# Performance work log

Measured on AMD Instinct MI355X. Metric: run time of the kernel, lower is better.

Reference implementation:

```python
import jax, jax.numpy as jnp
import numpy as np

N_NODES = 50000
N_EDGES = 800000
NODE_DIM = 128
EDGE_DIM = 16
OUT_DIM = 64
HEADS = 4


def setup_inputs() -> dict:
    key = jax.random.key(0)
    ks = jax.random.split(key, 12)
    x = jax.random.normal(ks[0], (N_NODES, NODE_DIM), jnp.float32)
    edge_index = jax.random.randint(ks[1], (2, N_EDGES), 0, N_NODES)
    batch = jnp.zeros((N_NODES,), jnp.int32)
    edge_attr = jax.random.normal(ks[2], (N_EDGES, EDGE_DIM), jnp.float32)
    s = 1.0 / np.sqrt(NODE_DIM)
    W = jax.random.normal(ks[3], (NODE_DIM, HEADS * OUT_DIM), jnp.float32) * s
    att_src = jax.random.normal(ks[4], (HEADS, OUT_DIM), jnp.float32) * 0.1
    att_dst = jax.random.normal(ks[5], (HEADS, OUT_DIM), jnp.float32) * 0.1
    W_e = jax.random.normal(ks[6], (EDGE_DIM, HEADS * OUT_DIM), jnp.float32) * (1.0 / np.sqrt(EDGE_DIM))
    att_edge = jax.random.normal(ks[7], (HEADS, OUT_DIM), jnp.float32) * 0.1
    bias = jnp.zeros((OUT_DIM,), jnp.float32)
    gamma = jnp.ones((OUT_DIM,), jnp.float32)
    beta = jnp.zeros((OUT_DIM,), jnp.float32)
    return {"x": x, "edge_index": edge_index, "batch": batch, "edge_attr": edge_attr,
            "W": W, "att_src": att_src, "att_dst": att_dst, "W_e": W_e,
            "att_edge": att_edge, "bias": bias, "gamma": gamma, "beta": beta}


def reference(x, edge_index, batch, edge_attr, W, att_src, att_dst, W_e, att_edge, bias, gamma, beta):
    N = x.shape[0]
    H, C = att_src.shape
    src, dst = edge_index[0], edge_index[1]
    E = src.shape[0]

    # add self loops; self-loop edge_attr = per-node mean of incoming edge attrs (PyG fill_value='mean')
    cnt = jax.ops.segment_sum(jnp.ones((E, 1), x.dtype), dst, num_segments=N)
    loop_attr = jax.ops.segment_sum(edge_attr, dst, num_segments=N) / jnp.maximum(cnt, 1.0)
    loop_idx = jnp.arange(N, dtype=src.dtype)
    src_f = jnp.concatenate([src, loop_idx])
    dst_f = jnp.concatenate([dst, loop_idx])
    ea = jnp.concatenate([edge_attr, loop_attr], axis=0)

    h = (x @ W).reshape(N, H, C)                       # [N,H,C]
    a_src = jnp.einsum('nhc,hc->nh', h, att_src)       # [N,H]
    a_dst = jnp.einsum('nhc,hc->nh', h, att_dst)
    e_emb = (ea @ W_e).reshape(-1, H, C)               # [E',H,C]
    a_edge = jnp.einsum('ehc,hc->eh', e_emb, att_edge)

    alpha = jax.nn.leaky_relu(a_src[src_f] + a_dst[dst_f] + a_edge, 0.2)  # [E',H]
    amax = jax.ops.segment_max(alpha, dst_f, num_segments=N)
    expa = jnp.exp(alpha - amax[dst_f])
    denom = jax.ops.segment_sum(expa, dst_f, num_segments=N)
    att = expa / (denom[dst_f] + 1e-16)                # segment softmax over dst

    msg = h[src_f] * att[:, :, None]                   # [E',H,C]
    out = jax.ops.segment_sum(msg, dst_f, num_segments=N)  # [N,H,C]
    out = out.mean(axis=1) + bias                      # concat=False -> head mean

    mu = out.mean(-1, keepdims=True)
    var = out.var(-1, keepdims=True)
    out = (out - mu) / jnp.sqrt(var + 1e-5) * gamma + beta
    return jax.nn.elu(out)
```

## Files before the change

### kernel.cpp

```cpp
#include <hip/hip_runtime.h>

typedef unsigned int u32;
typedef unsigned short u16;

static constexpr int NN  = 50000;
static constexpr int EE  = 800000;
static constexpr int CAP = 64;

typedef __attribute__((ext_vector_type(8))) short bf16x8;
typedef __attribute__((ext_vector_type(4))) float f32x4;

__device__ inline float u2f(u32 u){ union{u32 i; float f;} v; v.i=u; return v.f; }
__device__ inline float bf2f(u16 u){ return u2f(((u32)u)<<16); }
__device__ inline u16 f2bf(float f){ union{float f; u32 i;} v; v.f=f; u32 i=v.i;
    return (u16)((i + 0x7fffu + ((i>>16)&1u))>>16); }
__device__ inline float lrelu(float x){ return x > 0.f ? x : 0.2f*x; }

__device__ inline float ld(const void* base, size_t i, int f32m){
    return f32m ? ((const float*)base)[i] : bf2f(((const u16*)base)[i]);
}

__device__ inline float wsum(float v){
    #pragma unroll
    for (int m=1;m<64;m<<=1) v += __shfl_xor(v, m, 64);
    return v;
}
__device__ inline float wmax(float v){
    #pragma unroll
    for (int m=1;m<64;m<<=1) v = fmaxf(v, __shfl_xor(v, m, 64));
    return v;
}

__device__ inline int detect_f32(const u16* xraw){
    int lane = threadIdx.x & 63;
    bool bad = false;
    #pragma unroll
    for (int i = 0; i < 8; ++i){
        float v = bf2f(xraw[2*(lane + i*64)]);
        if (!(fabsf(v) < 1e10f)) bad = true;
    }
    return __any(bad) ? 1 : 0;
}

__global__ __launch_bounds__(256) void k_prep(const u16* __restrict__ xraw,
                                              const void* __restrict__ W,
                                              const void* __restrict__ att_src,
                                              const void* __restrict__ att_dst,
                                              const void* __restrict__ W_e,
                                              const void* __restrict__ att_edge,
                                              int* __restrict__ flag,
                                              u16* __restrict__ Wt,
                                              float* __restrict__ Mv){
    int f32m = detect_f32(xraw);
    int b = blockIdx.x, t = threadIdx.x;
    if (b == 0){
        if (t == 0) *flag = f32m;
        if (t < 64){
            int d = t >> 2, h = t & 3;
            float s = 0.f;
            for (int c = 0; c < 64; ++c)
                s += ld(W_e, d*256 + h*64 + c, f32m) * ld(att_edge, h*64 + c, f32m);
            Mv[t] = s;
        }
    } else if (b <= 128){
        int i = (b-1)*256 + t;
        int k = i >> 8, n = i & 255;
        Wt[n*128 + k] = f2bf(ld(W, (size_t)k*256 + n, f32m));
    } else {
        int i = (b-129)*256 + t;
        int c = i >> 7, k = i & 127;
        float s = 0.f;
        if (c < 8){
            int h = c & 3;
            const void* att = (c < 4) ? att_src : att_dst;
            for (int j = 0; j < 64; ++j)
                s += ld(W, (size_t)k*256 + h*64 + j, f32m) * ld(att, h*64 + j, f32m);
        }
        Wt[(size_t)(256 + c)*128 + k] = f2bf(s);
    }
}

__global__ __launch_bounds__(256) void k_edge(const int* __restrict__ ei,
                                              const void* __restrict__ ea,
                                              const float* __restrict__ Mv,
                                              const int* __restrict__ flag,
                                              int* __restrict__ deg,
                                              int* __restrict__ bsrc,
                                              uint2* __restrict__ bae, int E){
    __shared__ float Ml[64];
    if (threadIdx.x < 64) Ml[threadIdx.x] = Mv[threadIdx.x];
    __syncthreads();
    int e = blockIdx.x*256 + threadIdx.x;
    if (e >= E) return;
    int f32m = *flag;
    float v[16];
    if (f32m){
        const float4* r = ((const float4*)ea) + (size_t)e*4;
        float4 a = r[0], b = r[1], c = r[2], d = r[3];
        v[0]=a.x; v[1]=a.y; v[2]=a.z; v[3]=a.w;
        v[4]=b.x; v[5]=b.y; v[6]=b.z; v[7]=b.w;
        v[8]=c.x; v[9]=c.y; v[10]=c.z; v[11]=c.w;
        v[12]=d.x; v[13]=d.y; v[14]=d.z; v[15]=d.w;
    } else {
        const uint4* r = ((const uint4*)ea) + (size_t)e*2;
        uint4 q0 = r[0], q1 = r[1];
        v[0]=u2f(q0.x<<16); v[1]=u2f(q0.x&0xffff0000u);
        v[2]=u2f(q0.y<<16); v[3]=u2f(q0.y&0xffff0000u);
        v[4]=u2f(q0.z<<16); v[5]=u2f(q0.z&0xffff0000u);
        v[6]=u2f(q0.w<<16); v[7]=u2f(q0.w&0xffff0000u);
        v[8]=u2f(q1.x<<16); v[9]=u2f(q1.x&0xffff0000u);
        v[10]=u2f(q1.y<<16); v[11]=u2f(q1.y&0xffff0000u);
        v[12]=u2f(q1.z<<16); v[13]=u2f(q1.z&0xffff0000u);
        v[14]=u2f(q1.w<<16); v[15]=u2f(q1.w&0xffff0000u);
    }
    float a0=0,a1=0,a2=0,a3=0;
    #pragma unroll
    for (int j = 0; j < 16; ++j){
        a0 = fmaf(v[j], Ml[j*4+0], a0);
        a1 = fmaf(v[j], Ml[j*4+1], a1);
        a2 = fmaf(v[j], Ml[j*4+2], a2);
        a3 = fmaf(v[j], Ml[j*4+3], a3);
    }
    int src = ei[e], dst = ei[E + e];
    int slot = atomicAdd(&deg[dst], 1);
    if (slot < CAP){
        bsrc[dst*CAP + slot] = src;
        u32 lo = (u32)f2bf(a0) | ((u32)f2bf(a1)<<16);
        u32 hi = (u32)f2bf(a2) | ((u32)f2bf(a3)<<16);
        bae[dst*CAP + slot] = make_uint2(lo, hi);
    }
}

static constexpr int LDSROW = 136;
static constexpr int CROW   = 264;

__global__ __launch_bounds__(256) void k_gemm(const void* __restrict__ x,
                                              const u16* __restrict__ Wt,
                                              const int* __restrict__ flag,
                                              u16* __restrict__ hbuf,
                                              float* __restrict__ a_src,
                                              float* __restrict__ a_dst, int N){
    __shared__ u16 sh[64*CROW];
    int f32m = *flag;
    int t = threadIdx.x;
    int row0 = blockIdx.x*64;
    if (f32m){
        const float4* xg = (const float4*)x;
        #pragma unroll
        for (int j=0;j<8;++j){
            int idx = t + j*256;
            int r = idx >> 5, c4 = idx & 31;
            int gr = row0 + r; if (gr >= N) gr = N-1;
            float4 v = xg[(size_t)gr*32 + c4];
            u32 p0 = (u32)f2bf(v.x) | ((u32)f2bf(v.y)<<16);
            u32 p1 = (u32)f2bf(v.z) | ((u32)f2bf(v.w)<<16);
            *(uint2*)&sh[r*LDSROW + c4*4] = make_uint2(p0,p1);
        }
    } else {
        const uint4* xg = (const uint4*)x;
        #pragma unroll
        for (int j=0;j<4;++j){
            int idx = t + j*256;
            int r = idx >> 4, c8 = idx & 15;
            int gr = row0 + r; if (gr >= N) gr = N-1;
            uint4 v = xg[(size_t)gr*16 + c8];
            *(uint4*)&sh[r*LDSROW + c8*8] = v;
        }
    }
    __syncthreads();
    int wave = t >> 6, lane = t & 63;
    int l15 = lane & 15, quad = lane >> 4;
    int mrow = wave*16 + l15;
    bf16x8 afr[4];
    #pragma unroll
    for (int s=0;s<4;++s)
        afr[s] = *(const bf16x8*)&sh[mrow*LDSROW + s*32 + quad*8];
    __syncthreads();
    f32x4 acc[17];
    #pragma unroll
    for (int tl=0;tl<17;++tl){
        f32x4 a = {0.f,0.f,0.f,0.f};
        #pragma unroll
        for (int s=0;s<4;++s){
            bf16x8 bfr = *(const bf16x8*)&Wt[(size_t)(tl*16 + l15)*128 + s*32 + quad*8];
            a = __builtin_amdgcn_mfma_f32_16x16x32_bf16(afr[s], bfr, a, 0, 0, 0);
        }
        acc[tl] = a;
    }
    int rbase = row0 + wave*16 + quad*4;
    #pragma unroll
    for (int r=0;r<4;++r){
        int gr = rbase + r;
        if (gr < N){
            if (l15 < 4)      a_src[gr*4 + l15]     = acc[16][r];
            else if (l15 < 8) a_dst[gr*4 + (l15-4)] = acc[16][r];
        }
    }
    #pragma unroll
    for (int r=0;r<4;++r){
        int row = wave*16 + quad*4 + r;
        #pragma unroll
        for (int tl=0;tl<4;++tl){
            u32 lo = (u32)f2bf(acc[tl  ][r]) | ((u32)f2bf(acc[tl+4 ][r])<<16);
            u32 hi = (u32)f2bf(acc[tl+8][r]) | ((u32)f2bf(acc[tl+12][r])<<16);
            *(uint2*)&sh[row*CROW + (tl*16 + l15)*4] = make_uint2(lo, hi);
        }
    }
    __syncthreads();
    uint4* h4 = (uint4*)hbuf;
    #pragma unroll
    for (int j=0;j<8;++j){
        int idx = t + j*256;
        int row = idx >> 5, c16 = idx & 31;
        if (row0 + row < N){
            uint4 v = *(const uint4*)&sh[row*CROW + c16*8];
            h4[(size_t)(row0 + row)*32 + c16] = v;
        }
    }
}

__device__ inline void accum8(float* acc, float4 w, uint4 v){
    acc[0] = fmaf(w.x, u2f(v.x<<16),         acc[0]);
    acc[1] = fmaf(w.y, u2f(v.x&0xffff0000u), acc[1]);
    acc[2] = fmaf(w.z, u2f(v.y<<16),         acc[2]);
    acc[3] = fmaf(w.w, u2f(v.y&0xffff0000u), acc[3]);
    acc[4] = fmaf(w.x, u2f(v.z<<16),         acc[4]);
    acc[5] = fmaf(w.y, u2f(v.z&0xffff0000u), acc[5]);
    acc[6] = fmaf(w.z, u2f(v.w<<16),         acc[6]);
    acc[7] = fmaf(w.w, u2f(v.w&0xffff0000u), acc[7]);
}

__global__ __launch_bounds__(256) void k_node(const int* __restrict__ deg,
                                              const int* __restrict__ bsrc,
                                              const uint2* __restrict__ bae,
                                              const float* __restrict__ a_src,
                                              const float* __restrict__ a_dst,
                                              const u16* __restrict__ hbuf,
                                              const void* __restrict__ bias,
                                              const void* __restrict__ gamma,
                                              const void* __restrict__ beta,
                                              const int* __restrict__ flag,
                                              void* __restrict__ out, int N){
    __shared__ float4 wls[4][CAP+2];
    __shared__ int    sls[4][CAP+2];
    int f32m = *flag;
    int lane = threadIdx.x & 63;
    int slot = threadIdx.x >> 6;
    int n = blockIdx.x*4 + slot;
    int dg = deg[n];
    int dc = dg < CAP ? dg : CAP;
    const float4* as4 = (const float4*)a_src;
    float4 ad = ((const float4*)a_dst)[n];
    float4 an = as4[n];
    bool v0 = lane < dc;
    int s0 = n;
    float ae[4] = {0.f,0.f,0.f,0.f};
    float al0[4] = {-1e30f,-1e30f,-1e30f,-1e30f};
    if (v0){
        s0 = bsrc[n*CAP + lane];
        uint2 p = bae[n*CAP + lane];
        ae[0] = u2f(p.x<<16); ae[1] = u2f(p.x&0xffff0000u);
        ae[2] = u2f(p.y<<16); ae[3] = u2f(p.y&0xffff0000u);
        float4 as = as4[s0];
        al0[0] = lrelu(as.x + ad.x + ae[0]);
        al0[1] = lrelu(as.y + ad.y + ae[1]);
        al0[2] = lrelu(as.z + ad.z + ae[2]);
        al0[3] = lrelu(as.w + ad.w + ae[3]);
    }
    float invd = 1.f / (float)(dg > 1 ? dg : 1);
    float aS[4];
    #pragma unroll
    for (int h=0;h<4;++h) aS[h] = wsum(ae[h]) * invd;
    float alS[4];
    alS[0] = lrelu(an.x + ad.x + aS[0]);
    alS[1] = lrelu(an.y + ad.y + aS[1]);
    alS[2] = lrelu(an.z + ad.z + aS[2]);
    alS[3] = lrelu(an.w + ad.w + aS[3]);
    float ex0[4], exS[4], inv[4];
    #pragma unroll
    for (int h = 0; h < 4; ++h){
        float mx = fmaxf(wmax(al0[h]), alS[h]);
        ex0[h] = v0 ? expf(al0[h] - mx) : 0.f;
        exS[h] = expf(alS[h] - mx);
        float s = wsum(ex0[h]) + exS[h];
        inv[h] = 1.f / (s + 1e-16f);
    }
    if (v0){
        wls[slot][lane] = make_float4(ex0[0]*inv[0], ex0[1]*inv[1], ex0[2]*inv[2], ex0[3]*inv[3]);
        sls[slot][lane] = s0;
    }
    if (lane == 0){
        wls[slot][dc]   = make_float4(exS[0]*inv[0], exS[1]*inv[1], exS[2]*inv[2], exS[3]*inv[3]);
        sls[slot][dc]   = n;
        wls[slot][dc+1] = make_float4(0.f,0.f,0.f,0.f);
        sls[slot][dc+1] = n;
    }
    __syncthreads();
    int T = dc + 1;
    int pairs = (T + 1) >> 1;
    int half = lane >> 5, l5 = lane & 31;
    const uint4* hb4 = (const uint4*)hbuf;
    float acc[8] = {0,0,0,0,0,0,0,0};
    int t = 0;
    for (; t + 2 <= pairs; t += 2){
        int ja = 2*t + half, jb = 2*t + 2 + half;
        int sa = sls[slot][ja], sb = sls[slot][jb];
        float4 wa = wls[slot][ja], wb = wls[slot][jb];
        uint4 va = hb4[(size_t)sa*32 + l5];
        uint4 vb = hb4[(size_t)sb*32 + l5];
        accum8(acc, wa, va);
        accum8(acc, wb, vb);
    }
    for (; t < pairs; ++t){
        int j = 2*t + half;
        int s = sls[slot][j];
        float4 w = wls[slot][j];
        uint4 v = hb4[(size_t)s*32 + l5];
        accum8(acc, w, v);
    }
    float oc0 = 0.25f*(acc[0]+acc[1]+acc[2]+acc[3]);
    float oc1 = 0.25f*(acc[4]+acc[5]+acc[6]+acc[7]);
    oc0 += __shfl_xor(oc0, 32, 64);
    oc1 += __shfl_xor(oc1, 32, 64);
    float va = __shfl(oc0, lane>>1, 64);
    float vb = __shfl(oc1, lane>>1, 64);
    float o = ((lane & 1) ? vb : va) + ld(bias, lane, f32m);
    float mu = wsum(o) * (1.f/64.f);
    float d = o - mu;
    float var = wsum(d*d) * (1.f/64.f);
    float y = d * rsqrtf(var + 1e-5f) * ld(gamma, lane, f32m) + ld(beta, lane, f32m);
    y = y > 0.f ? y : expf(y) - 1.f;
    if (f32m) ((float*)out)[(size_t)n*64 + lane] = y;
    else      ((u16*)out)[(size_t)n*64 + lane] = f2bf(y);
}

extern "C" void kernel_launch(void* const* d_in, const int* in_sizes, int n_in,
                              void* d_out, int out_size, void* d_ws, size_t ws_size,
                              hipStream_t stream){
    const void* x        = d_in[0];
    const int*  ei       = (const int*)d_in[1];
    const void* ea       = d_in[3];
    const void* W        = d_in[4];
    const void* att_src  = d_in[5];
    const void* att_dst  = d_in[6];
    const void* W_e      = d_in[7];
    const void* att_edge = d_in[8];
    const void* bias     = d_in[9];
    const void* gamma    = d_in[10];
    const void* beta     = d_in[11];
    const int N = NN, E = EE;

    char* p = (char*)d_ws;
    auto alloc = [&](size_t bytes){ void* r = (void*)p; p += (bytes + 255) & ~(size_t)255; return r; };
    int*   deg   = (int*)  alloc((size_t)N*4);
    int*   bsrc  = (int*)  alloc((size_t)N*CAP*4);
    uint2* bae   = (uint2*)alloc((size_t)N*CAP*8);
    float* Mv    = (float*)alloc(64*4);
    float* a_src = (float*)alloc((size_t)N*16);
    float* a_dst = (float*)alloc((size_t)N*16);
    u16*   hbuf  = (u16*)  alloc((size_t)N*256*2);
    u16*   Wt    = (u16*)  alloc((size_t)272*128*2);
    int*   flag  = (int*)  alloc(256);

    hipMemsetAsync(deg, 0, (size_t)N*4, stream);
    k_prep<<<137, 256, 0, stream>>>((const u16*)x, W, att_src, att_dst, W_e, att_edge,
                                    flag, Wt, Mv);
    k_edge<<<(E+255)/256, 256, 0, stream>>>(ei, ea, Mv, flag, deg, bsrc, bae, E);
    k_gemm<<<(N+63)/64, 256, 0, stream>>>(x, Wt, flag, hbuf, a_src, a_dst, N);
    k_node<<<N/4, 256, 0, stream>>>(deg, bsrc, bae, a_src, a_dst, hbuf,
                                    bias, gamma, beta, flag, d_out, N);
}
```

Measured before the change: 305.6 us.

## Compute unnormalized softmax weights per edge with atomic denominators, simplify node aggregation

Reorders the kernels so the node GEMM runs before the edge pass. The edge kernel then computes exp(leaky_relu) attention weights directly, without subtracting a max. It accumulates per-destination denominators and edge-attribute sums with float atomics and stores packed src and bf16 weight records. The node kernel drops its wave-wide max and sum reductions, rescales the stored weights, and aggregates with bf16 dot2 instructions. The trade is removing the segment-max stabilization and reduction work at the cost of eight scattered float atomics per edge, plus possible overflow for large logits.

```diff
diff --git a/kernel.cpp b/kernel.cpp
--- a/kernel.cpp
+++ b/kernel.cpp
@@ -14,6 +14,7 @@
 __device__ inline float bf2f(u16 u){ return u2f(((u32)u)<<16); }
 __device__ inline u16 f2bf(float f){ union{float f; u32 i;} v; v.f=f; u32 i=v.i;
     return (u16)((i + 0x7fffu + ((i>>16)&1u))>>16); }
+__device__ inline u32 pk2(float a, float b){ return (u32)f2bf(a) | ((u32)f2bf(b)<<16); }
 __device__ inline float lrelu(float x){ return x > 0.f ? x : 0.2f*x; }
 
 __device__ inline float ld(const void* base, size_t i, int f32m){
@@ -25,10 +26,26 @@
     for (int m=1;m<64;m<<=1) v += __shfl_xor(v, m, 64);
     return v;
 }
-__device__ inline float wmax(float v){
-    #pragma unroll
-    for (int m=1;m<64;m<<=1) v = fmaxf(v, __shfl_xor(v, m, 64));
-    return v;
+
+#if defined(__has_builtin)
+#if __has_builtin(__builtin_amdgcn_fdot2_f32_bf16)
+#define HAS_DOT2 1
+#endif
+#endif
+
+#ifdef HAS_DOT2
+typedef __attribute__((ext_vector_type(2))) __bf16 bf16x2;
+#endif
+
+__device__ inline float dot2acc(u32 hv, u32 wv, float acc){
+#ifdef HAS_DOT2
+    union { u32 u; bf16x2 v; } a, b; a.u = hv; b.u = wv;
+    return __builtin_amdgcn_fdot2_f32_bf16(a.v, b.v, acc, false);
+#else
+    acc = fmaf(u2f(hv<<16),         u2f(wv<<16),         acc);
+    acc = fmaf(u2f(hv&0xffff0000u), u2f(wv&0xffff0000u), acc);
+    return acc;
+#endif
 }
 
 __device__ inline int detect_f32(const u16* xraw){
@@ -80,13 +97,102 @@
     }
 }
 
+static constexpr int LDSROW = 136;
+static constexpr int CROW   = 264;
+
+__global__ __launch_bounds__(256) void k_gemm(const void* __restrict__ x,
+                                              const u16* __restrict__ Wt,
+                                              const int* __restrict__ flag,
+                                              u16* __restrict__ hbuf,
+                                              float* __restrict__ a_src,
+                                              float* __restrict__ a_dst, int N){
+    __shared__ u16 sh[64*CROW];
+    int f32m = *flag;
+    int t = threadIdx.x;
+    int row0 = blockIdx.x*64;
+    if (f32m){
+        const float4* xg = (const float4*)x;
+        #pragma unroll
+        for (int j=0;j<8;++j){
+            int idx = t + j*256;
+            int r = idx >> 5, c4 = idx & 31;
+            int gr = row0 + r; if (gr >= N) gr = N-1;
+            float4 v = xg[(size_t)gr*32 + c4];
+            *(uint2*)&sh[r*LDSROW + c4*4] = make_uint2(pk2(v.x,v.y), pk2(v.z,v.w));
+        }
+    } else {
+        const uint4* xg = (const uint4*)x;
+        #pragma unroll
+        for (int j=0;j<4;++j){
+            int idx = t + j*256;
+            int r = idx >> 4, c8 = idx & 15;
+            int gr = row0 + r; if (gr >= N) gr = N-1;
+            uint4 v = xg[(size_t)gr*16 + c8];
+            *(uint4*)&sh[r*LDSROW + c8*8] = v;
+        }
+    }
+    __syncthreads();
+    int wave = t >> 6, lane = t & 63;
+    int l15 = lane & 15, quad = lane >> 4;
+    int mrow = wave*16 + l15;
+    bf16x8 afr[4];
+    #pragma unroll
+    for (int s=0;s<4;++s)
+        afr[s] = *(const bf16x8*)&sh[mrow*LDSROW + s*32 + quad*8];
+    __syncthreads();
+    f32x4 acc[17];
+    #pragma unroll
+    for (int tl=0;tl<17;++tl){
+        f32x4 a = {0.f,0.f,0.f,0.f};
+        #pragma unroll
+        for (int s=0;s<4;++s){
+            bf16x8 bfr = *(const bf16x8*)&Wt[(size_t)(tl*16 + l15)*128 + s*32 + quad*8];
+            a = __builtin_amdgcn_mfma_f32_16x16x32_bf16(afr[s], bfr, a, 0, 0, 0);
+        }
+        acc[tl] = a;
+    }
+    int rbase = row0 + wave*16 + quad*4;
+    #pragma unroll
+    for (int r=0;r<4;++r){
+        int gr = rbase + r;
+        if (gr < N){
+            if (l15 < 4)      a_src[gr*4 + l15]     = acc[16][r];
+            else if (l15 < 8) a_dst[gr*4 + (l15-4)] = acc[16][r];
+        }
+    }
+    #pragma unroll
+    for (int r=0;r<4;++r){
+        int row = wave*16 + quad*4 + r;
+        #pragma unroll
+        for (int tl=0;tl<4;++tl){
+            u32 lo = pk2(acc[tl  ][r], acc[tl+4 ][r]);
+            u32 hi = pk2(acc[tl+8][r], acc[tl+12][r]);
+            *(uint2*)&sh[row*CROW + (tl*16 + l15)*4] = make_uint2(lo, hi);
+        }
+    }
+    __syncthreads();
+    uint4* h4 = (uint4*)hbuf;
+    #pragma unroll
+    for (int j=0;j<8;++j){
+        int idx = t + j*256;
+        int row = idx >> 5, c16 = idx & 31;
+        if (row0 + row < N){
+            uint4 v = *(const uint4*)&sh[row*CROW + c16*8];
+            h4[(size_t)(row0 + row)*32 + c16] = v;
+        }
+    }
+}
+
 __global__ __launch_bounds__(256) void k_edge(const int* __restrict__ ei,
                                               const void* __restrict__ ea,
                                               const float* __restrict__ Mv,
                                               const int* __restrict__ flag,
+                                              const float* __restrict__ a_src,
+                                              const float* __restrict__ a_dst,
                                               int* __restrict__ deg,
-                                              int* __restrict__ bsrc,
-                                              uint2* __restrict__ bae, int E){
+                                              float* __restrict__ denom,
+                                              float* __restrict__ aesum,
+                                              uint4* __restrict__ brec, int E){
     __shared__ float Ml[64];
     if (threadIdx.x < 64) Ml[threadIdx.x] = Mv[threadIdx.x];
     __syncthreads();
@@ -122,208 +228,92 @@
         a3 = fmaf(v[j], Ml[j*4+3], a3);
     }
     int src = ei[e], dst = ei[E + e];
+    float4 as = ((const float4*)a_src)[src];
+    float4 ad = ((const float4*)a_dst)[dst];
+    float w0 = expf(lrelu(as.x + ad.x + a0));
+    float w1 = expf(lrelu(as.y + ad.y + a1));
+    float w2 = expf(lrelu(as.z + ad.z + a2));
+    float w3 = expf(lrelu(as.w + ad.w + a3));
+    atomicAdd(&denom[dst*4+0], w0);
+    atomicAdd(&denom[dst*4+1], w1);
+    atomicAdd(&denom[dst*4+2], w2);
+    atomicAdd(&denom[dst*4+3], w3);
+    atomicAdd(&aesum[dst*4+0], a0);
+    atomicAdd(&aesum[dst*4+1], a1);
+    atomicAdd(&aesum[dst*4+2], a2);
+    atomicAdd(&aesum[dst*4+3], a3);
     int slot = atomicAdd(&deg[dst], 1);
-    if (slot < CAP){
-        bsrc[dst*CAP + slot] = src;
-        u32 lo = (u32)f2bf(a0) | ((u32)f2bf(a1)<<16);
-        u32 hi = (u32)f2bf(a2) | ((u32)f2bf(a3)<<16);
-        bae[dst*CAP + slot] = make_uint2(lo, hi);
-    }
-}
-
-static constexpr int LDSROW = 136;
-static constexpr int CROW   = 264;
-
-__global__ __launch_bounds__(256) void k_gemm(const void* __restrict__ x,
-                                              const u16* __restrict__ Wt,
-                                              const int* __restrict__ flag,
-                                              u16* __restrict__ hbuf,
-                                              float* __restrict__ a_src,
-                                              float* __restrict__ a_dst, int N){
-    __shared__ u16 sh[64*CROW];
-    int f32m = *flag;
-    int t = threadIdx.x;
-    int row0 = blockIdx.x*64;
-    if (f32m){
-        const float4* xg = (const float4*)x;
-        #pragma unroll
-        for (int j=0;j<8;++j){
-            int idx = t + j*256;
-            int r = idx >> 5, c4 = idx & 31;
-            int gr = row0 + r; if (gr >= N) gr = N-1;
-            float4 v = xg[(size_t)gr*32 + c4];
-            u32 p0 = (u32)f2bf(v.x) | ((u32)f2bf(v.y)<<16);
-            u32 p1 = (u32)f2bf(v.z) | ((u32)f2bf(v.w)<<16);
-            *(uint2*)&sh[r*LDSROW + c4*4] = make_uint2(p0,p1);
-        }
-    } else {
-        const uint4* xg = (const uint4*)x;
-        #pragma unroll
-        for (int j=0;j<4;++j){
-            int idx = t + j*256;
-            int r = idx >> 4, c8 = idx & 15;
-            int gr = row0 + r; if (gr >= N) gr = N-1;
-            uint4 v = xg[(size_t)gr*16 + c8];
-            *(uint4*)&sh[r*LDSROW + c8*8] = v;
-        }
-    }
-    __syncthreads();
-    int wave = t >> 6, lane = t & 63;
-    int l15 = lane & 15, quad = lane >> 4;
-    int mrow = wave*16 + l15;
-    bf16x8 afr[4];
-    #pragma unroll
-    for (int s=0;s<4;++s)
-        afr[s] = *(const bf16x8*)&sh[mrow*LDSROW + s*32 + quad*8];
-    __syncthreads();
-    f32x4 acc[17];
-    #pragma unroll
-    for (int tl=0;tl<17;++tl){
-        f32x4 a = {0.f,0.f,0.f,0.f};
-        #pragma unroll
-        for (int s=0;s<4;++s){
-            bf16x8 bfr = *(const bf16x8*)&Wt[(size_t)(tl*16 + l15)*128 + s*32 + quad*8];
-            a = __builtin_amdgcn_mfma_f32_16x16x32_bf16(afr[s], bfr, a, 0, 0, 0);
-        }
-        acc[tl] = a;
-    }
-    int rbase = row0 + wave*16 + quad*4;
-    #pragma unroll
-    for (int r=0;r<4;++r){
-        int gr = rbase + r;
-        if (gr < N){
-            if (l15 < 4)      a_src[gr*4 + l15]     = acc[16][r];
-            else if (l15 < 8) a_dst[gr*4 + (l15-4)] = acc[16][r];
-        }
-    }
-    #pragma unroll
-    for (int r=0;r<4;++r){
-        int row = wave*16 + quad*4 + r;
-        #pragma unroll
-        for (int tl=0;tl<4;++tl){
-            u32 lo = (u32)f2bf(acc[tl  ][r]) | ((u32)f2bf(acc[tl+4 ][r])<<16);
-            u32 hi = (u32)f2bf(acc[tl+8][r]) | ((u32)f2bf(acc[tl+12][r])<<16);
-            *(uint2*)&sh[row*CROW + (tl*16 + l15)*4] = make_uint2(lo, hi);
-        }
-    }
-    __syncthreads();
-    uint4* h4 = (uint4*)hbuf;
-    #pragma unroll
-    for (int j=0;j<8;++j){
-        int idx = t + j*256;
-        int row = idx >> 5, c16 = idx & 31;
-        if (row0 + row < N){
-            uint4 v = *(const uint4*)&sh[row*CROW + c16*8];
-            h4[(size_t)(row0 + row)*32 + c16] = v;
-        }
-    }
-}
-
-__device__ inline void accum8(float* acc, float4 w, uint4 v){
-    acc[0] = fmaf(w.x, u2f(v.x<<16),         acc[0]);
-    acc[1] = fmaf(w.y, u2f(v.x&0xffff0000u), acc[1]);
-    acc[2] = fmaf(w.z, u2f(v.y<<16),         acc[2]);
-    acc[3] = fmaf(w.w, u2f(v.y&0xffff0000u), acc[3]);
-    acc[4] = fmaf(w.x, u2f(v.z<<16),         acc[4]);
-    acc[5] = fmaf(w.y, u2f(v.z&0xffff0000u), acc[5]);
-    acc[6] = fmaf(w.z, u2f(v.w<<16),         acc[6]);
-    acc[7] = fmaf(w.w, u2f(v.w&0xffff0000u), acc[7]);
+    if (slot < CAP)
+        brec[dst*CAP + slot] = make_uint4((u32)src, pk2(w0,w1), pk2(w2,w3), 0u);
 }
 
 __global__ __launch_bounds__(256) void k_node(const int* __restrict__ deg,
-                                              const int* __restrict__ bsrc,
-                                              const uint2* __restrict__ bae,
+                                              const float* __restrict__ denom,
+                                              const float* __restrict__ aesum,
                                               const float* __restrict__ a_src,
                                               const float* __restrict__ a_dst,
+                                              const uint4* __restrict__ brec,
                                               const u16* __restrict__ hbuf,
                                               const void* __restrict__ bias,
                                               const void* __restrict__ gamma,
                                               const void* __restrict__ beta,
                                               const int* __restrict__ flag,
                                               void* __restrict__ out, int N){
-    __shared__ float4 wls[4][CAP+2];
-    __shared__ int    sls[4][CAP+2];
+    __shared__ uint4 lrec[4][CAP+4];
     int f32m = *flag;
     int lane = threadIdx.x & 63;
     int slot = threadIdx.x >> 6;
     int n = blockIdx.x*4 + slot;
     int dg = deg[n];
     int dc = dg < CAP ? dg : CAP;
-    const float4* as4 = (const float4*)a_src;
+    float4 dn = ((const float4*)denom)[n];
+    float4 ge = ((const float4*)aesum)[n];
+    float4 an = ((const float4*)a_src)[n];
     float4 ad = ((const float4*)a_dst)[n];
-    float4 an = as4[n];
-    bool v0 = lane < dc;
-    int s0 = n;
-    float ae[4] = {0.f,0.f,0.f,0.f};
-    float al0[4] = {-1e30f,-1e30f,-1e30f,-1e30f};
-    if (v0){
-        s0 = bsrc[n*CAP + lane];
-        uint2 p = bae[n*CAP + lane];
-        ae[0] = u2f(p.x<<16); ae[1] = u2f(p.x&0xffff0000u);
-        ae[2] = u2f(p.y<<16); ae[3] = u2f(p.y&0xffff0000u);
-        float4 as = as4[s0];
-        al0[0] = lrelu(as.x + ad.x + ae[0]);
-        al0[1] = lrelu(as.y + ad.y + ae[1]);
-        al0[2] = lrelu(as.z + ad.z + ae[2]);
-        al0[3] = lrelu(as.w + ad.w + ae[3]);
-    }
     float invd = 1.f / (float)(dg > 1 ? dg : 1);
-    float aS[4];
-    #pragma unroll
-    for (int h=0;h<4;++h) aS[h] = wsum(ae[h]) * invd;
-    float alS[4];
-    alS[0] = lrelu(an.x + ad.x + aS[0]);
-    alS[1] = lrelu(an.y + ad.y + aS[1]);
-    alS[2] = lrelu(an.z + ad.z + aS[2]);
-    alS[3] = lrelu(an.w + ad.w + aS[3]);
-    float ex0[4], exS[4], inv[4];
-    #pragma unroll
-    for (int h = 0; h < 4; ++h){
-        float mx = fmaxf(wmax(al0[h]), alS[h]);
-        ex0[h] = v0 ? expf(al0[h] - mx) : 0.f;
-        exS[h] = expf(alS[h] - mx);
-        float s = wsum(ex0[h]) + exS[h];
-        inv[h] = 1.f / (s + 1e-16f);
-    }
-    if (v0){
-        wls[slot][lane] = make_float4(ex0[0]*inv[0], ex0[1]*inv[1], ex0[2]*inv[2], ex0[3]*inv[3]);
-        sls[slot][lane] = s0;
-    }
-    if (lane == 0){
-        wls[slot][dc]   = make_float4(exS[0]*inv[0], exS[1]*inv[1], exS[2]*inv[2], exS[3]*inv[3]);
-        sls[slot][dc]   = n;
-        wls[slot][dc+1] = make_float4(0.f,0.f,0.f,0.f);
-        sls[slot][dc+1] = n;
-    }
+    float exS0 = expf(lrelu(an.x + ad.x + ge.x*invd));
+    float exS1 = expf(lrelu(an.y + ad.y + ge.y*invd));
+    float exS2 = expf(lrelu(an.z + ad.z + ge.z*invd));
+    float exS3 = expf(lrelu(an.w + ad.w + ge.w*invd));
+    float i0 = 0.25f/(dn.x + exS0 + 1e-16f);
+    float i1 = 0.25f/(dn.y + exS1 + 1e-16f);
+    float i2 = 0.25f/(dn.z + exS2 + 1e-16f);
+    float i3 = 0.25f/(dn.w + exS3 + 1e-16f);
+    if (lane < dc){
+        uint4 r = brec[(size_t)n*CAP + lane];
+        float w0 = u2f(r.y<<16)*i0, w1 = u2f(r.y&0xffff0000u)*i1;
+        float w2 = u2f(r.z<<16)*i2, w3 = u2f(r.z&0xffff0000u)*i3;
+        lrec[slot][lane] = make_uint4(r.x, pk2(w0,w1), pk2(w2,w3), 0u);
+    }
+    if (lane == 0)
+        lrec[slot][dc] = make_uint4((u32)n, pk2(exS0*i0, exS1*i1), pk2(exS2*i2, exS3*i3), 0u);
+    else if (lane <= 3)
+        lrec[slot][dc + lane] = make_uint4((u32)n, 0u, 0u, 0u);
     __syncthreads();
     int T = dc + 1;
-    int pairs = (T + 1) >> 1;
+    int iters = (T + 3) >> 2;
     int half = lane >> 5, l5 = lane & 31;
     const uint4* hb4 = (const uint4*)hbuf;
-    float acc[8] = {0,0,0,0,0,0,0,0};
-    int t = 0;
-    for (; t + 2 <= pairs; t += 2){
-        int ja = 2*t + half, jb = 2*t + 2 + half;
-        int sa = sls[slot][ja], sb = sls[slot][jb];
-        float4 wa = wls[slot][ja], wb = wls[slot][jb];
-        uint4 va = hb4[(size_t)sa*32 + l5];
-        uint4 vb = hb4[(size_t)sb*32 + l5];
-        accum8(acc, wa, va);
-        accum8(acc, wb, vb);
-    }
-    for (; t < pairs; ++t){
-        int j = 2*t + half;
-        int s = sls[slot][j];
-        float4 w = wls[slot][j];
-        uint4 v = hb4[(size_t)s*32 + l5];
-        accum8(acc, w, v);
-    }
-    float oc0 = 0.25f*(acc[0]+acc[1]+acc[2]+acc[3]);
-    float oc1 = 0.25f*(acc[4]+acc[5]+acc[6]+acc[7]);
-    oc0 += __shfl_xor(oc0, 32, 64);
-    oc1 += __shfl_xor(oc1, 32, 64);
-    float va = __shfl(oc0, lane>>1, 64);
-    float vb = __shfl(oc1, lane>>1, 64);
+    float acc0 = 0.f, acc1 = 0.f;
+    for (int i = 0; i < iters; ++i){
+        int j0 = 4*i + half, j1 = j0 + 2;
+        uint4 r0 = lrec[slot][j0];
+        uint4 r1 = lrec[slot][j1];
+        uint4 v0 = hb4[(size_t)r0.x*32 + l5];
+        uint4 v1 = hb4[(size_t)r1.x*32 + l5];
+        acc0 = dot2acc(v0.x, r0.y, acc0);
+        acc0 = dot2acc(v0.y, r0.z, acc0);
+        acc1 = dot2acc(v0.z, r0.y, acc1);
+        acc1 = dot2acc(v0.w, r0.z, acc1);
+        acc0 = dot2acc(v1.x, r1.y, acc0);
+        acc0 = dot2acc(v1.y, r1.z, acc0);
+        acc1 = dot2acc(v1.z, r1.y, acc1);
+        acc1 = dot2acc(v1.w, r1.z, acc1);
+    }
+    acc0 += __shfl_xor(acc0, 32, 64);
+    acc1 += __shfl_xor(acc1, 32, 64);
+    float va = __shfl(acc0, lane>>1, 64);
+    float vb = __shfl(acc1, lane>>1, 64);
     float o = ((lane & 1) ? vb : va) + ld(bias, lane, f32m);
     float mu = wsum(o) * (1.f/64.f);
     float d = o - mu;
@@ -353,20 +343,23 @@
     char* p = (char*)d_ws;
     auto alloc = [&](size_t bytes){ void* r = (void*)p; p += (bytes + 255) & ~(size_t)255; return r; };
     int*   deg   = (int*)  alloc((size_t)N*4);
-    int*   bsrc  = (int*)  alloc((size_t)N*CAP*4);
-    uint2* bae   = (uint2*)alloc((size_t)N*CAP*8);
+    float* denom = (float*)alloc((size_t)N*16);
+    float* aesum = (float*)alloc((size_t)N*16);
+    size_t zbytes = (size_t)((char*)p - (char*)deg);
     float* Mv    = (float*)alloc(64*4);
     float* a_src = (float*)alloc((size_t)N*16);
     float* a_dst = (float*)alloc((size_t)N*16);
+    uint4* brec  = (uint4*)alloc((size_t)N*CAP*16);
     u16*   hbuf  = (u16*)  alloc((size_t)N*256*2);
     u16*   Wt    = (u16*)  alloc((size_t)272*128*2);
     int*   flag  = (int*)  alloc(256);
 
-    hipMemsetAsync(deg, 0, (size_t)N*4, stream);
+    hipMemsetAsync(deg, 0, zbytes, stream);
     k_prep<<<137, 256, 0, stream>>>((const u16*)x, W, att_src, att_dst, W_e, att_edge,
                                     flag, Wt, Mv);
-    k_edge<<<(E+255)/256, 256, 0, stream>>>(ei, ea, Mv, flag, deg, bsrc, bae, E);
     k_gemm<<<(N+63)/64, 256, 0, stream>>>(x, Wt, flag, hbuf, a_src, a_dst, N);
-    k_node<<<N/4, 256, 0, stream>>>(deg, bsrc, bae, a_src, a_dst, hbuf,
+    k_edge<<<(E+255)/256, 256, 0, stream>>>(ei, ea, Mv, flag, a_src, a_dst,
+                                            deg, denom, aesum, brec, E);
+    k_node<<<N/4, 256, 0, stream>>>(deg, denom, aesum, a_src, a_dst, brec, hbuf,
                                     bias, gamma, beta, flag, d_out, N);
 }
```

Measured after the change: 584.5 us. 91.2% more time.
